# Performance work log

Hardware: AMD Instinct MI355X
Metric: run time of the kernel (lower is better)

Reference implementation:

```python
import jax, jax.numpy as jnp
import numpy as np

HIDDEN = 1152
PATCH = 16
POS_SIZE = 64
B = 16
NP_ = 4096
IN_DIM = 3 * PATCH * PATCH  # 768


def setup_inputs() -> dict:
    key = jax.random.key(0)
    k1, k2, k3, k4, k5 = jax.random.split(key, 5)
    pixel_values = jax.random.normal(k1, (B, NP_, IN_DIM), dtype=jnp.float32)
    pixel_position_ids = jax.random.randint(k2, (B, NP_, 2), 0, POS_SIZE, dtype=jnp.int64)
    padding_positions = jax.random.randint(k3, (B, NP_), 0, 2) > 0
    # learned params: nn.Linear(input_dim, hidden, bias=False) weight is [hidden, in_dim]
    W = jax.random.normal(k4, (HIDDEN, IN_DIM), dtype=jnp.float32) / np.sqrt(IN_DIM)
    table = jax.random.normal(k5, (2, POS_SIZE, HIDDEN), dtype=jnp.float32)
    return {
        "pixel_values": pixel_values,
        "pixel_position_ids": pixel_position_ids,
        "padding_positions": padding_positions,
        "W": W,
        "table": table,
    }


def reference(pixel_values, pixel_position_ids, padding_positions, W, table):
    # input_proj: [B, N, in_dim] @ W.T -> [B, N, hidden]
    hidden_states = jnp.einsum("bnd,hd->bnh", pixel_values, W)
    # one_hot + matmul + sum over axis-of-2 is exactly a gather of the x-row
    # from table[0] plus the y-row from table[1]
    pos = jnp.clip(pixel_position_ids, 0, None)  # [B, N, 2]
    pe = table[0][pos[..., 0]] + table[1][pos[..., 1]]  # [B, N, hidden]
    pe = jnp.where(padding_positions[..., None], jnp.zeros_like(pe), pe)
    return hidden_states + pe
```

## Files before the change

kernel.cpp:

```cpp
#include <hip/hip_runtime.h>
#include <hip/hip_bf16.h>

#define HIDDEN 1152
#define IN_DIM 768
#define POS_SIZE 64
#define M_TOTAL (16 * 4096)

#define BM 128
#define BN 128
#define BK 32
#define NTILES (HIDDEN / BN)

typedef _Float16 f16x8 __attribute__((ext_vector_type(8)));
typedef float f32x4 __attribute__((ext_vector_type(4)));
typedef float f32x8v __attribute__((ext_vector_type(8)));

typedef __attribute__((address_space(1))) const void global_cv;
typedef __attribute__((address_space(3))) void lds_v;

__device__ __forceinline__ void async16(const void* g, void* l) {
    __builtin_amdgcn_global_load_lds((global_cv*)g, (lds_v*)l, 16, 0, 0);
}

__global__ __launch_bounds__(256) void cvt_f32_f16(const float* __restrict__ in,
                                                   _Float16* __restrict__ out, int n8) {
    int i = blockIdx.x * 256 + threadIdx.x;
    int stride = gridDim.x * 256;
    for (; i < n8; i += stride) {
        f32x8v x = ((const f32x8v*)in)[i];
        f16x8 h = __builtin_convertvector(x, f16x8);
        ((f16x8*)out)[i] = h;
    }
}

__global__ __launch_bounds__(256) void gemm_pe(const _Float16* __restrict__ A,
                                               const _Float16* __restrict__ Wh,
                                               const int* __restrict__ pos,
                                               const int* __restrict__ pad,
                                               const float* __restrict__ table,
                                               float* __restrict__ out) {
    __shared__ _Float16 sA[BM * BK];
    __shared__ _Float16 sB[BN * BK];

    const int bid = blockIdx.x;
    const int mt = bid / NTILES;
    const int nt = bid - mt * NTILES;
    const int m0 = mt * BM;
    const int n0 = nt * BN;

    const int t = threadIdx.x;
    const int lane = t & 63;
    const int w = t >> 6;
    const int quad = lane >> 4;
    const int l15 = lane & 15;
    const int wm = (w >> 1) * 64;
    const int wn = (w & 1) * 64;

    const int c0 = t, c1 = t + 256;
    const int ar0 = c0 >> 2, ac0 = (c0 & 3) * 8;
    const int ar1 = c1 >> 2, ac1 = (c1 & 3) * 8;

    const _Float16* gA = A + (size_t)m0 * IN_DIM;
    const _Float16* gB = Wh + (size_t)n0 * IN_DIM;

    f32x4 acc[4][4];
#pragma unroll
    for (int i = 0; i < 4; i++)
#pragma unroll
        for (int j = 0; j < 4; j++) acc[i][j] = (f32x4)0.f;

    for (int k0 = 0; k0 < IN_DIM; k0 += BK) {
        async16(gA + (size_t)ar0 * IN_DIM + k0 + ac0, &sA[c0 * 8]);
        async16(gA + (size_t)ar1 * IN_DIM + k0 + ac1, &sA[c1 * 8]);
        async16(gB + (size_t)ar0 * IN_DIM + k0 + ac0, &sB[c0 * 8]);
        async16(gB + (size_t)ar1 * IN_DIM + k0 + ac1, &sB[c1 * 8]);
        __syncthreads();

        f16x8 af[4], bf[4];
#pragma unroll
        for (int mi = 0; mi < 4; mi++)
            af[mi] = *(const f16x8*)&sA[(wm + mi * 16 + l15) * BK + quad * 8];
#pragma unroll
        for (int ni = 0; ni < 4; ni++)
            bf[ni] = *(const f16x8*)&sB[(wn + ni * 16 + l15) * BK + quad * 8];

#pragma unroll
        for (int mi = 0; mi < 4; mi++)
#pragma unroll
            for (int ni = 0; ni < 4; ni++)
                acc[mi][ni] = __builtin_amdgcn_mfma_f32_16x16x32_f16(af[mi], bf[ni],
                                                                     acc[mi][ni], 0, 0, 0);
        __syncthreads();
    }

    const float* t0 = table;
    const float* t1 = table + POS_SIZE * HIDDEN;
#pragma unroll
    for (int mi = 0; mi < 4; mi++) {
#pragma unroll
        for (int r = 0; r < 4; r++) {
            const int gm = m0 + wm + mi * 16 + quad * 4 + r;
            int px = pos[gm * 2];
            int py = pos[gm * 2 + 1];
            px = px < 0 ? 0 : px;
            py = py < 0 ? 0 : py;
            const int isPad = pad[gm];
            const float* rx = t0 + (size_t)px * HIDDEN;
            const float* ry = t1 + (size_t)py * HIDDEN;
            float* orow = out + (size_t)gm * HIDDEN;
#pragma unroll
            for (int ni = 0; ni < 4; ni++) {
                const int gn = n0 + wn + ni * 16 + l15;
                float pe = isPad ? 0.f : (rx[gn] + ry[gn]);
                orow[gn] = acc[mi][ni][r] + pe;
            }
        }
    }
}

__global__ __launch_bounds__(256) void fallback_naive(const float* __restrict__ A,
                                                      const float* __restrict__ W,
                                                      const int* __restrict__ pos,
                                                      const int* __restrict__ pad,
                                                      const float* __restrict__ table,
                                                      float* __restrict__ out) {
    long idx = (long)blockIdx.x * 256 + threadIdx.x;
    const long total = (long)M_TOTAL * HIDDEN;
    if (idx >= total) return;
    int m = (int)(idx / HIDDEN);
    int n = (int)(idx - (long)m * HIDDEN);
    const float* a = A + (size_t)m * IN_DIM;
    const float* wv = W + (size_t)n * IN_DIM;
    float s = 0.f;
    for (int k = 0; k < IN_DIM; k++) s += a[k] * wv[k];
    int px = pos[m * 2]; if (px < 0) px = 0;
    int py = pos[m * 2 + 1]; if (py < 0) py = 0;
    float pe = pad[m] ? 0.f : (table[(size_t)px * HIDDEN + n] +
                               table[(size_t)(POS_SIZE + py) * HIDDEN + n]);
    out[idx] = s + pe;
}

extern "C" void kernel_launch(void* const* d_in, const int* in_sizes, int n_in,
                              void* d_out, int out_size, void* d_ws, size_t ws_size,
                              hipStream_t stream) {
    const float* pixel = (const float*)d_in[0];
    const int* pos = (const int*)d_in[1];
    const int* pad = (const int*)d_in[2];
    const float* W = (const float*)d_in[3];
    const float* table = (const float*)d_in[4];
    float* out = (float*)d_out;

    const size_t nA = (size_t)M_TOTAL * IN_DIM;
    const size_t nW = (size_t)HIDDEN * IN_DIM;
    const size_t need = (nA + nW) * sizeof(_Float16);

    if (ws_size >= need) {
        _Float16* Ah = (_Float16*)d_ws;
        _Float16* Whh = Ah + nA;
        cvt_f32_f16<<<4096, 256, 0, stream>>>(pixel, Ah, (int)(nA / 8));
        cvt_f32_f16<<<432, 256, 0, stream>>>(W, Whh, (int)(nW / 8));
        gemm_pe<<<(M_TOTAL / BM) * NTILES, 256, 0, stream>>>(Ah, Whh, pos, pad, table, out);
    } else {
        long total = (long)M_TOTAL * HIDDEN;
        fallback_naive<<<(int)((total + 255) / 256), 256, 0, stream>>>(pixel, W, pos, pad,
                                                                       table, out);
    }
}
```

Measured before the change: 661.1 us.

## Fuse pixel fp32-to-fp16 conversion into GEMM with full-K LDS row tiles

Drops the separate fp32-to-fp16 conversion pass over the large pixel tensor. Each block now loads a 64-row slab of fp32 pixels once, converts it into padded LDS, and walks all 1152 output columns against it. W is pre-packed into an MFMA-fragment layout so B fragments come straight from global memory/cache with register double-buffering. This removes one full read and write of the activation matrix, at the cost of heavy LDS use (one block per CU), no overlap between the A load and compute, and B traffic going through cache rather than LDS.

Measured after the change: 1.124 ms. 1.7x slower.

```diff
diff --git a/kernel.cpp b/kernel.cpp
--- a/kernel.cpp
+++ b/kernel.cpp
@@ -1,118 +1,127 @@
 #include <hip/hip_runtime.h>
-#include <hip/hip_bf16.h>
 
 #define HIDDEN 1152
 #define IN_DIM 768
 #define POS_SIZE 64
 #define M_TOTAL (16 * 4096)
 
-#define BM 128
-#define BN 128
-#define BK 32
-#define NTILES (HIDDEN / BN)
+#define BM 64
+#define KSTEPS 24
+#define LDA 776
 
 typedef _Float16 f16x8 __attribute__((ext_vector_type(8)));
 typedef float f32x4 __attribute__((ext_vector_type(4)));
 typedef float f32x8v __attribute__((ext_vector_type(8)));
 
-typedef __attribute__((address_space(1))) const void global_cv;
-typedef __attribute__((address_space(3))) void lds_v;
-
-__device__ __forceinline__ void async16(const void* g, void* l) {
-    __builtin_amdgcn_global_load_lds((global_cv*)g, (lds_v*)l, 16, 0, 0);
+__global__ __launch_bounds__(256) void pack_w(const float* __restrict__ W,
+                                              _Float16* __restrict__ Wp) {
+    unsigned tid = blockIdx.x * 256 + threadIdx.x;
+    unsigned n = tid / 96u;
+    unsigned kc = tid - n * 96u;
+    f32x8v x = *(const f32x8v*)(W + (size_t)n * IN_DIM + kc * 8u);
+    f16x8 h = __builtin_convertvector(x, f16x8);
+    unsigned c = (n >> 4) * 1536u + kc * 16u + (n & 15u);
+    ((f16x8*)Wp)[c] = h;
 }
 
-__global__ __launch_bounds__(256) void cvt_f32_f16(const float* __restrict__ in,
-                                                   _Float16* __restrict__ out, int n8) {
-    int i = blockIdx.x * 256 + threadIdx.x;
-    int stride = gridDim.x * 256;
-    for (; i < n8; i += stride) {
-        f32x8v x = ((const f32x8v*)in)[i];
-        f16x8 h = __builtin_convertvector(x, f16x8);
-        ((f16x8*)out)[i] = h;
-    }
+__device__ __forceinline__ void load_frags(const _Float16* sA, const f16x8* pw,
+                                           int l15, int quad, int ntc, int ks,
+                                           f16x8 af[4], f16x8 bb[3][2]) {
+#pragma unroll
+    for (int mi = 0; mi < 4; mi++)
+        af[mi] = *(const f16x8*)&sA[(mi * 16 + l15) * LDA + ks * 32 + quad * 8];
+#pragma unroll
+    for (int j = 0; j < 3; j++)
+#pragma unroll
+        for (int ni = 0; ni < 2; ni++)
+            bb[j][ni] = pw[(size_t)(ntc + j) * 12288 + ni * 1536 + ks * 64];
 }
 
-__global__ __launch_bounds__(256) void gemm_pe(const _Float16* __restrict__ A,
-                                               const _Float16* __restrict__ Wh,
-                                               const int* __restrict__ pos,
-                                               const int* __restrict__ pad,
-                                               const float* __restrict__ table,
-                                               float* __restrict__ out) {
-    __shared__ _Float16 sA[BM * BK];
-    __shared__ _Float16 sB[BN * BK];
+__device__ __forceinline__ void do_mfma(const f16x8 af[4], const f16x8 bb[3][2],
+                                        f32x4 acc[3][4][2]) {
+#pragma unroll
+    for (int j = 0; j < 3; j++)
+#pragma unroll
+        for (int mi = 0; mi < 4; mi++)
+#pragma unroll
+            for (int ni = 0; ni < 2; ni++)
+                acc[j][mi][ni] = __builtin_amdgcn_mfma_f32_16x16x32_f16(
+                    af[mi], bb[j][ni], acc[j][mi][ni], 0, 0, 0);
+}
 
-    const int bid = blockIdx.x;
-    const int mt = bid / NTILES;
-    const int nt = bid - mt * NTILES;
-    const int m0 = mt * BM;
-    const int n0 = nt * BN;
+__global__ __launch_bounds__(256, 1) void gemm_pe(
+    const float* __restrict__ A,
+    const _Float16* __restrict__ Wp,
+    const int* __restrict__ pos,
+    const int* __restrict__ pad,
+    const float* __restrict__ table,
+    float* __restrict__ out) {
+    __shared__ _Float16 sA[BM * LDA];
 
+    const int m0 = blockIdx.x * BM;
     const int t = threadIdx.x;
     const int lane = t & 63;
     const int w = t >> 6;
     const int quad = lane >> 4;
     const int l15 = lane & 15;
-    const int wm = (w >> 1) * 64;
-    const int wn = (w & 1) * 64;
 
-    const int c0 = t, c1 = t + 256;
-    const int ar0 = c0 >> 2, ac0 = (c0 & 3) * 8;
-    const int ar1 = c1 >> 2, ac1 = (c1 & 3) * 8;
+    {
+        const float* gA = A + (size_t)m0 * IN_DIM;
+#pragma unroll 4
+        for (int i = 0; i < 24; i++) {
+            int c = t + i * 256;
+            int row = c / 96;
+            int col8 = c - row * 96;
+            f32x8v x = *(const f32x8v*)(gA + (size_t)row * IN_DIM + col8 * 8);
+            f16x8 h = __builtin_convertvector(x, f16x8);
+            *(f16x8*)&sA[row * LDA + col8 * 8] = h;
+        }
+    }
+    __syncthreads();
 
-    const _Float16* gA = A + (size_t)m0 * IN_DIM;
-    const _Float16* gB = Wh + (size_t)n0 * IN_DIM;
+    const f16x8* pw = (const f16x8*)Wp + (size_t)(w * 2) * 1536 + lane;
 
-    f32x4 acc[4][4];
+    for (int ntc = 0; ntc < 9; ntc += 3) {
+        f32x4 acc[3][4][2];
 #pragma unroll
-    for (int i = 0; i < 4; i++)
+        for (int j = 0; j < 3; j++)
 #pragma unroll
-        for (int j = 0; j < 4; j++) acc[i][j] = (f32x4)0.f;
+            for (int mi = 0; mi < 4; mi++)
+#pragma unroll
+                for (int ni = 0; ni < 2; ni++) acc[j][mi][ni] = (f32x4)0.f;
 
-    for (int k0 = 0; k0 < IN_DIM; k0 += BK) {
-        async16(gA + (size_t)ar0 * IN_DIM + k0 + ac0, &sA[c0 * 8]);
-        async16(gA + (size_t)ar1 * IN_DIM + k0 + ac1, &sA[c1 * 8]);
-        async16(gB + (size_t)ar0 * IN_DIM + k0 + ac0, &sB[c0 * 8]);
-        async16(gB + (size_t)ar1 * IN_DIM + k0 + ac1, &sB[c1 * 8]);
-        __syncthreads();
-
-        f16x8 af[4], bf[4];
-#pragma unroll
-        for (int mi = 0; mi < 4; mi++)
-            af[mi] = *(const f16x8*)&sA[(wm + mi * 16 + l15) * BK + quad * 8];
-#pragma unroll
-        for (int ni = 0; ni < 4; ni++)
-            bf[ni] = *(const f16x8*)&sB[(wn + ni * 16 + l15) * BK + quad * 8];
+        f16x8 afA[4], afB[4], bA[3][2], bB[3][2];
+        load_frags(sA, pw, l15, quad, ntc, 0, afA, bA);
+        for (int ks = 0; ks < KSTEPS; ks += 2) {
+            load_frags(sA, pw, l15, quad, ntc, ks + 1, afB, bB);
+            do_mfma(afA, bA, acc);
+            if (ks + 2 < KSTEPS) load_frags(sA, pw, l15, quad, ntc, ks + 2, afA, bA);
+            do_mfma(afB, bB, acc);
+        }
 
 #pragma unroll
-        for (int mi = 0; mi < 4; mi++)
+        for (int j = 0; j < 3; j++) {
+            const int gn0 = (ntc + j) * 128 + w * 32;
 #pragma unroll
-            for (int ni = 0; ni < 4; ni++)
-                acc[mi][ni] = __builtin_amdgcn_mfma_f32_16x16x32_f16(af[mi], bf[ni],
-                                                                     acc[mi][ni], 0, 0, 0);
-        __syncthreads();
-    }
-
-    const float* t0 = table;
-    const float* t1 = table + POS_SIZE * HIDDEN;
+            for (int mi = 0; mi < 4; mi++) {
 #pragma unroll
-    for (int mi = 0; mi < 4; mi++) {
+                for (int r = 0; r < 4; r++) {
+                    const int gm = m0 + mi * 16 + quad * 4 + r;
+                    int px = pos[gm * 2];
+                    int py = pos[gm * 2 + 1];
+                    px = px < 0 ? 0 : px;
+                    py = py < 0 ? 0 : py;
+                    const int isPad = pad[gm];
+                    const float* rx = table + (size_t)px * HIDDEN;
+                    const float* ry = table + (size_t)(POS_SIZE + py) * HIDDEN;
+                    float* orow = out + (size_t)gm * HIDDEN;
 #pragma unroll
-        for (int r = 0; r < 4; r++) {
-            const int gm = m0 + wm + mi * 16 + quad * 4 + r;
-            int px = pos[gm * 2];
-            int py = pos[gm * 2 + 1];
-            px = px < 0 ? 0 : px;
-            py = py < 0 ? 0 : py;
-            const int isPad = pad[gm];
-            const float* rx = t0 + (size_t)px * HIDDEN;
-            const float* ry = t1 + (size_t)py * HIDDEN;
-            float* orow = out + (size_t)gm * HIDDEN;
-#pragma unroll
-            for (int ni = 0; ni < 4; ni++) {
-                const int gn = n0 + wn + ni * 16 + l15;
-                float pe = isPad ? 0.f : (rx[gn] + ry[gn]);
-                orow[gn] = acc[mi][ni][r] + pe;
+                    for (int ni = 0; ni < 2; ni++) {
+                        const int gn = gn0 + ni * 16 + l15;
+                        float pe = isPad ? 0.f : (rx[gn] + ry[gn]);
+                        orow[gn] = acc[j][mi][ni][r] + pe;
+                    }
+                }
             }
         }
     }
@@ -150,16 +159,11 @@
     const float* table = (const float*)d_in[4];
     float* out = (float*)d_out;
 
-    const size_t nA = (size_t)M_TOTAL * IN_DIM;
     const size_t nW = (size_t)HIDDEN * IN_DIM;
-    const size_t need = (nA + nW) * sizeof(_Float16);
-
-    if (ws_size >= need) {
-        _Float16* Ah = (_Float16*)d_ws;
-        _Float16* Whh = Ah + nA;
-        cvt_f32_f16<<<4096, 256, 0, stream>>>(pixel, Ah, (int)(nA / 8));
-        cvt_f32_f16<<<432, 256, 0, stream>>>(W, Whh, (int)(nW / 8));
-        gemm_pe<<<(M_TOTAL / BM) * NTILES, 256, 0, stream>>>(Ah, Whh, pos, pad, table, out);
+    if (ws_size >= nW * sizeof(_Float16)) {
+        _Float16* Wp = (_Float16*)d_ws;
+        pack_w<<<432, 256, 0, stream>>>(W, Wp);
+        gemm_pe<<<M_TOTAL / BM, 256, 0, stream>>>(pixel, Wp, pos, pad, table, out);
     } else {
         long total = (long)M_TOTAL * HIDDEN;
         fallback_naive<<<(int)((total + 255) / 256), 256, 0, stream>>>(pixel, W, pos, pad,
```
